# Kernel tuning notes

Measured on AMD Instinct MI355X. Metric: run time of the kernel, lower is better.

Reference implementation:

```python
import jax, jax.numpy as jnp
import numpy as np

B, S, C = 4, 1024, 1024
HD = 64          # hard-coded head dim in the module
H = C // HD      # 16 heads
ROT = 32         # RotaryEmbedding hard-codes Dim=32 (partial rotary)
EPS = 1e-4       # pnormalize eps


def pnormalize(w, parts):
    # torch: reshape(parts, -1, *w.shape[1:]); vector_norm over trailing dims;
    # alpha = sqrt(n.numel()/partitioned.numel()) = 1/sqrt(fan_in); w / (eps + alpha*n)
    p = w.reshape(parts, -1, w.shape[-1])
    n = jnp.linalg.norm(p, axis=-1, keepdims=True)
    alpha = np.sqrt(n.size / p.size)
    return (p / (EPS + alpha * n)).reshape(w.shape)


def mp_linear(x, w, parts):
    fan_in = w.shape[-1]
    return x @ (pnormalize(w, parts) / np.sqrt(fan_in)).T


def rotate_half(t):
    t1, t2 = jnp.split(t, 2, axis=-1)
    return jnp.concatenate([-t2, t1], axis=-1)


def apply_rope(t, freqs):
    return t * jnp.cos(freqs) + rotate_half(t) * jnp.sin(freqs)


def setup_inputs() -> dict:
    key = jax.random.key(0)
    k1, k2, k3, k4 = jax.random.split(key, 4)
    x = jax.random.normal(k1, (B, S, C), jnp.float32)
    w_qkv = jax.random.normal(k2, (3 * C, C), jnp.float32)   # MPLinear init: std=1
    w_out = jax.random.normal(k3, (C, C), jnp.float32)
    sink = jax.random.normal(k4, (1, 1, C), jnp.float32)
    # rotary table: RotaryEmbedding with Dim=32
    inv_freq = 1.0 / (10000.0 ** (np.arange(0, ROT, 2, dtype=np.float32) / ROT))
    t = np.arange(S, dtype=np.float32)
    freqs = np.einsum('i,j->ij', t, inv_freq)          # (S, 16)
    re = jnp.asarray(np.concatenate([freqs, freqs], axis=-1)[None, None], jnp.float32)  # (1,1,S,32)
    # causal mask over S+1 tokens (sink appended last); sink row/col fully visible
    Sf = S + 1
    m = np.tril(np.ones((Sf, Sf), dtype=bool))
    m[:, -1] = True
    m[-1, :] = True
    attn_mask = jnp.asarray(m)
    return {"x": x, "re": re, "attn_mask": attn_mask, "w_qkv": w_qkv, "w_out": w_out, "sink": sink}


def reference(x, re, attn_mask, w_qkv, w_out, sink):
    Bn, Sn, Cn = x.shape
    Hn = Cn // HD
    # append sink token
    x = jnp.concatenate([x, jnp.broadcast_to(sink, (Bn, 1, Cn))], axis=1)  # (B, S+1, C)
    qkv = mp_linear(x, w_qkv, 3)
    q, k, v = jnp.split(qkv, 3, axis=-1)
    scale = HD ** (-0.25)
    heads = lambda t: t.reshape(Bn, -1, Hn, HD).transpose(0, 2, 1, 3)  # (B,H,S+1,64)
    q, k, v = heads(q * scale), heads(k * scale), heads(v)
    # partial rotary: only non-sink tokens, only first ROT dims of head
    q_s, k_s = q[:, :, -1:], k[:, :, -1:]
    qb, kb = q[:, :, :-1], k[:, :, :-1]
    l = re.shape[-1]
    qb = jnp.concatenate([apply_rope(qb[..., :l], re), qb[..., l:]], axis=-1)
    kb = jnp.concatenate([apply_rope(kb[..., :l], re), kb[..., l:]], axis=-1)
    q = jnp.concatenate([qb, q_s], axis=2)
    k = jnp.concatenate([kb, k_s], axis=2)
    # cosine attention: unit-normalize q, k over head dim
    q = q / jnp.linalg.norm(q, axis=-1, keepdims=True)
    k = k / jnp.linalg.norm(k, axis=-1, keepdims=True)
    M = jnp.einsum('bhid,bhjd->bhij', q, k)  # (B,H,S+1,S+1)
    Sf = q.shape[2]
    M = jnp.where(attn_mask[None, None, :Sf, :Sf], M, -jnp.inf)
    A = jax.nn.softmax(M, axis=-1)
    h = jnp.einsum('bhij,bhjd->bhid', A, v)
    h = h[:, :, :-1]  # drop sink output
    h = h.transpose(0, 2, 1, 3).reshape(Bn, Sn, Cn)
    # mag_norm (no-grad magnitude matching against post-sink input x)
    desired = jax.lax.stop_gradient(jnp.mean(jnp.linalg.norm(x, axis=-1)))
    current = jax.lax.stop_gradient(jnp.mean(jnp.linalg.norm(h, axis=-1)))
    h = h * (desired / current)
    return mp_linear(h, w_out, 1)
```

## Files before the change

### kernel.cpp

```cpp
#include <hip/hip_runtime.h>
#include <hip/hip_bf16.h>
#include <cstdint>

typedef __attribute__((ext_vector_type(8))) short short8;
typedef __attribute__((ext_vector_type(4))) float f32x4;

typedef const unsigned int __attribute__((address_space(1)))* gas_ptr;
typedef unsigned int __attribute__((address_space(3)))* las_ptr;

__device__ static inline void async16(const void* g, void* l) {
  __builtin_amdgcn_global_load_lds((gas_ptr)g, (las_ptr)l, 16, 0, 0);
}

__device__ static inline unsigned short f2bf(float f) {
  union { float f; uint32_t u; } v; v.f = f;
  uint32_t u = v.u;
  uint32_t r = (u + 0x7FFFu + ((u >> 16) & 1u)) >> 16;
  return (unsigned short)r;
}
__device__ static inline float bf2f(unsigned short s) {
  union { uint32_t u; float f; } v; v.u = ((uint32_t)s) << 16; return v.f;
}

__device__ static inline float wave_sum(float v) {
  v += __shfl_xor(v, 1);  v += __shfl_xor(v, 2);  v += __shfl_xor(v, 4);
  v += __shfl_xor(v, 8);  v += __shfl_xor(v, 16); v += __shfl_xor(v, 32);
  return v;
}

#define SBAR __builtin_amdgcn_sched_barrier(0)

__global__ __launch_bounds__(256) void k_prep(const float* __restrict__ x,
    const float* __restrict__ sink, const float* __restrict__ re,
    const float* __restrict__ w_qkv, const float* __restrict__ w_out,
    unsigned short* __restrict__ Xe, unsigned short* __restrict__ Wq,
    unsigned short* __restrict__ Wo,
    float* __restrict__ ctT, float* __restrict__ stT, float* __restrict__ rowsn) {
  __shared__ float red[4];
  const int bid = blockIdx.x;
  const int tid = threadIdx.x, w = tid >> 6, l = tid & 63;
  if (bid < 4224) {
    const int row = bid;
    const int c4 = tid * 4;
    float4 v = make_float4(0.f, 0.f, 0.f, 0.f);
    if (row < 4100) {
      int b = row / 1025, s = row - b * 1025;
      const float* src = (s < 1024) ? (x + ((size_t)(b * 1024 + s)) * 1024 + c4) : (sink + c4);
      v = *(const float4*)src;
    }
    *(ushort4*)(Xe + (size_t)row * 1024 + c4) =
        make_ushort4(f2bf(v.x), f2bf(v.y), f2bf(v.z), f2bf(v.w));
    float ss = v.x * v.x + v.y * v.y + v.z * v.z + v.w * v.w;
    ss = wave_sum(ss);
    if (l == 0) red[w] = ss;
    __syncthreads();
    if (tid == 0) rowsn[row] = (row < 4100) ? sqrtf(red[0] + red[1] + red[2] + red[3]) : 0.f;
  } else if (bid < 4288) {
    int i = (bid - 4224) * 256 + tid;
    int s = i >> 4, r2 = i & 15;
    float f = re[s * 32 + r2];
    ctT[r2 * 1024 + s] = cosf(f);
    stT[r2 * 1024 + s] = sinf(f);
  } else {
    const float* W; unsigned short* E; int row;
    if (bid < 5056) { W = w_qkv; E = Wq; row = (bid - 4288) * 4 + w; }
    else            { W = w_out; E = Wo; row = (bid - 5056) * 4 + w; }
    const float* wr = W + (size_t)row * 1024;
    float4 v[4];
    float s = 0.f;
    #pragma unroll
    for (int i = 0; i < 4; ++i) {
      v[i] = *(const float4*)(wr + i * 256 + l * 4);
      s += v[i].x * v[i].x + v[i].y * v[i].y + v[i].z * v[i].z + v[i].w * v[i].w;
    }
    s = wave_sum(s);
    float inv = 1.0f / (0.0032f + sqrtf(s));
    unsigned short* er = E + (size_t)row * 1024;
    #pragma unroll
    for (int i = 0; i < 4; ++i) {
      ushort4 o = make_ushort4(f2bf(v[i].x * inv), f2bf(v[i].y * inv),
                               f2bf(v[i].z * inv), f2bf(v[i].w * inv));
      *(ushort4*)(er + i * 256 + l * 4) = o;
    }
  }
}

__global__ __launch_bounds__(256) void k_rownormC(const float* __restrict__ rowsqp,
    const float* __restrict__ rowsn, float* __restrict__ scp) {
  __shared__ float red[4];
  const int bid = blockIdx.x, t = threadIdx.x, w = t >> 6, l = t & 63;
  const int row = bid * 256 + t;
  const float4* rp = (const float4*)(rowsqp + (size_t)row * 16);
  float4 a = rp[0], b = rp[1], c = rp[2], d = rp[3];
  float s = a.x + a.y + a.z + a.w + b.x + b.y + b.z + b.w +
            c.x + c.y + c.z + c.w + d.x + d.y + d.z + d.w;
  float v = sqrtf(s);
  v = wave_sum(v);
  if (l == 0) red[w] = v;
  __syncthreads();
  if (t == 0) scp[16 + bid] = red[0] + red[1] + red[2] + red[3];
  float u = 0.f;
  for (int k = t; k < 264; k += 256) u += rowsn[bid * 264 + k];
  u = wave_sum(u);
  __syncthreads();
  if (l == 0) red[w] = u;
  __syncthreads();
  if (t == 0) scp[bid] = red[0] + red[1] + red[2] + red[3];
}

template<int EPI>
__global__ __launch_bounds__(256, 4) void k_gemm128(
    const unsigned short* __restrict__ A, const unsigned short* __restrict__ B,
    float* __restrict__ C, int N, int K, int ntn,
    unsigned short* __restrict__ Qh, unsigned short* __restrict__ Kh,
    unsigned short* __restrict__ Vt,
    const float* __restrict__ ctT, const float* __restrict__ stT,
    const float* __restrict__ scp) {
  constexpr int BM = EPI ? 128 : 64;
  constexpr int MI = BM / 32;
  __shared__ __align__(16) short SMEM[(BM + 128) * 64];
  short* Al = SMEM;
  short* Bl = SMEM + BM * 64;
  const int t = threadIdx.x, l = t & 63, w = t >> 6;
  const int r = l & 15, g = l >> 4;
  const int wm = w >> 1, wn = w & 1;
  const int nwg = gridDim.x;
  const int q = nwg >> 3, rr = nwg & 7;
  const int xcd = blockIdx.x & 7, loc = blockIdx.x >> 3;
  const int wgid = (xcd < rr ? xcd * (q + 1) : rr * (q + 1) + (xcd - rr) * q) + loc;
  const int tm = wgid / ntn, tn = wgid % ntn;
  const size_t am0 = (size_t)tm * BM, bn0 = (size_t)tn * 128;

  f32x4 acc[MI][4] = {};
  for (int kt = 0; kt < K; kt += 64) {
    __syncthreads();
    #pragma unroll
    for (int i = 0; i < BM / 32; ++i) {
      int c = i * 256 + t;
      int row = c >> 3, sch = (c & 7) ^ (row & 7);
      async16(A + (am0 + row) * (size_t)K + kt + sch * 8, Al + (i * 256 + w * 64) * 8);
    }
    #pragma unroll
    for (int i = 0; i < 4; ++i) {
      int c = i * 256 + t;
      int row = c >> 3, sch = (c & 7) ^ (row & 7);
      async16(B + (bn0 + row) * (size_t)K + kt + sch * 8, Bl + (i * 256 + w * 64) * 8);
    }
    __syncthreads();
    #pragma unroll
    for (int ks = 0; ks < 2; ++ks) {
      short8 af[MI], bfr[4];
      #pragma unroll
      for (int mi = 0; mi < MI; ++mi) {
        const int arow = wm * (MI * 16) + mi * 16 + r;
        af[mi] = *(const short8*)(Al + arow * 64 + (((ks * 4 + g) ^ (arow & 7)) << 3));
      }
      #pragma unroll
      for (int ni = 0; ni < 4; ++ni) {
        const int brow = wn * 64 + ni * 16 + r;
        bfr[ni] = *(const short8*)(Bl + brow * 64 + (((ks * 4 + g) ^ (brow & 7)) << 3));
      }
      #pragma unroll
      for (int mi = 0; mi < MI; ++mi)
        #pragma unroll
        for (int ni = 0; ni < 4; ++ni)
          acc[mi][ni] = __builtin_amdgcn_mfma_f32_16x16x32_bf16(af[mi], bfr[ni], acc[mi][ni], 0, 0, 0);
    }
  }

  if constexpr (EPI == 0) {
    float num = 0.f, den = 0.f;
    #pragma unroll
    for (int i = 0; i < 16; ++i) { num += scp[i]; den += scp[16 + i]; }
    const float ratio = (num * (1.0f / 4100.0f)) * (4096.0f / den);
    #pragma unroll
    for (int mi = 0; mi < MI; ++mi)
      #pragma unroll
      for (int ni = 0; ni < 4; ++ni)
        #pragma unroll
        for (int j = 0; j < 4; ++j) {
          size_t row = am0 + wm * (MI * 16) + mi * 16 + g * 4 + j;
          size_t col = bn0 + wn * 64 + ni * 16 + r;
          C[row * (size_t)N + col] = acc[mi][ni][j] * ratio;
        }
  } else {
    __syncthreads();
    const int head_global = tn * 2 + wn;
    const int sel = head_global >> 4;
    const int h = head_global & 15;
    const int row0 = (int)am0 + wm * 64;

    if (sel < 2) {
      unsigned short* dst = (sel == 0) ? Qh : Kh;
      #pragma unroll
      for (int mi = 0; mi < 4; ++mi) {
        const int rowb = row0 + mi * 16 + g * 4;
        const int b = rowb / 1025;
        const int s0 = rowb - b * 1025;
        float cs[4], sn[4];
        if (s0 + 3 < 1024) {
          float4 c4 = *(const float4*)(ctT + r * 1024 + s0);
          float4 s4 = *(const float4*)(stT + r * 1024 + s0);
          cs[0] = c4.x; cs[1] = c4.y; cs[2] = c4.z; cs[3] = c4.w;
          sn[0] = s4.x; sn[1] = s4.y; sn[2] = s4.z; sn[3] = s4.w;
        } else {
          #pragma unroll
          for (int j = 0; j < 4; ++j) {
            const int rj = rowb + j;
            const int bj = rj / 1025, sj = rj - bj * 1025;
            cs[j] = (sj < 1024) ? ctT[r * 1024 + sj] : 1.f;
            sn[j] = (sj < 1024) ? stT[r * 1024 + sj] : 0.f;
          }
        }
        #pragma unroll
        for (int j = 0; j < 4; ++j) {
          const int row = rowb + j;
          const int b2 = row / 1025, s = row - b2 * 1025;
          const float a0 = acc[mi][0][j], a1 = acc[mi][1][j];
          const float a2 = acc[mi][2][j], a3 = acc[mi][3][j];
          const float r0 = a0 * cs[j] - a1 * sn[j];
          const float r1 = a1 * cs[j] + a0 * sn[j];
          float nrm = r0 * r0 + r1 * r1 + a2 * a2 + a3 * a3;
          nrm += __shfl_xor(nrm, 1); nrm += __shfl_xor(nrm, 2);
          nrm += __shfl_xor(nrm, 4); nrm += __shfl_xor(nrm, 8);
          const float inv = rsqrtf(nrm);
          if (row < 4100) {
            const size_t base = ((size_t)(b2 * 16 + h) * 1088 + s) * 64 + r;
            dst[base]      = f2bf(r0 * inv);
            dst[base + 16] = f2bf(r1 * inv);
            dst[base + 32] = f2bf(a2 * inv);
            dst[base + 48] = f2bf(a3 * inv);
          }
        }
      }
    } else {
      short* vs = SMEM + w * 4096;
      #pragma unroll
      for (int mi = 0; mi < 4; ++mi) {
        const int slot = mi * 4 + g;
        #pragma unroll
        for (int ni = 0; ni < 4; ++ni) {
          const int d = ni * 16 + r;
          ushort4 pk = make_ushort4(f2bf(acc[mi][ni][0]), f2bf(acc[mi][ni][1]),
                                    f2bf(acc[mi][ni][2]), f2bf(acc[mi][ni][3]));
          *(ushort4*)(vs + d * 64 + ((slot ^ (d & 15)) << 2)) = pk;
        }
      }
      asm volatile("s_waitcnt lgkmcnt(0)" ::: "memory"); SBAR;
      #pragma unroll
      for (int ii = 0; ii < 16; ++ii) {
        const int d = ii * 4 + g;
        ushort4 vv = *(const ushort4*)(vs + d * 64 + (((r ^ (d & 15)) & 15) << 2));
        const int grow = row0 + r * 4;
        const int b0 = grow / 1025, b3 = (grow + 3) / 1025;
        if (b0 == b3 && grow + 3 < 4100) {
          const int s = grow - b0 * 1025;
          *(ushort4*)(Vt + ((size_t)(b0 * 16 + h) * 64 + d) * 1088 + s) = vv;
        } else {
          unsigned short tmp[4] = {vv.x, vv.y, vv.z, vv.w};
          for (int k2 = 0; k2 < 4; ++k2) {
            const int gr = grow + k2;
            if (gr >= 4100) break;
            const int bb = gr / 1025, ss = gr - bb * 1025;
            Vt[((size_t)(bb * 16 + h) * 64 + d) * 1088 + ss] = tmp[k2];
          }
        }
      }
    }
  }
}

__global__ __launch_bounds__(256) void k_attn(const unsigned short* __restrict__ Qh,
    const unsigned short* __restrict__ Kh, const unsigned short* __restrict__ Vt,
    unsigned short* __restrict__ Hb, float* __restrict__ rowsqp) {
  __shared__ __align__(16) short Kl[2][64 * 64];
  __shared__ __align__(16) short Vl[2][64 * 64];
  __shared__ __align__(16) short Pl[64 * 64];
  const int wid = blockIdx.x;
  const int xcd = wid & 7, jj = wid >> 3;
  const int bh = xcd + 8 * (jj & 7);
  const int p = 15 - (jj >> 3);
  const int b = bh >> 4, hh = bh & 15;
  const int t = threadIdx.x, l = t & 63, w = t >> 6;
  const int r = l & 15, g = l >> 4;
  const int qrow0 = p * 64 + w * 16;

  auto stage = [&](int buf, int kt) {
    #pragma unroll
    for (int i = 0; i < 2; ++i) {
      int c = i * 256 + t;
      int row = c >> 3, sch = (c & 7) ^ (row & 7);
      async16(Kh + ((size_t)bh * 1088 + kt * 64 + row) * 64 + sch * 8,
              Kl[buf] + (i * 256 + w * 64) * 8);
      async16(Vt + ((size_t)bh * 64 + row) * 1088 + kt * 64 + sch * 8,
              Vl[buf] + (i * 256 + w * 64) * 8);
    }
  };

  short8 qf[2];
  #pragma unroll
  for (int ks = 0; ks < 2; ++ks)
    qf[ks] = *(const short8*)(Qh + ((size_t)bh * 1088 + qrow0 + r) * 64 + ks * 32 + g * 8);
  f32x4 oacc[4] = {};
  float lsum[4] = {0.f, 0.f, 0.f, 0.f};
  stage(0, 0);
  __syncthreads();
  int cur = 0;
  for (int i = 0; i <= p; ++i) {
    if (i < p) stage(cur ^ 1, i + 1);
    const bool needmask = (i == p);
    for (int nc = 0; nc < 4; ++nc) {
      f32x4 sc = {};
      #pragma unroll
      for (int ks = 0; ks < 2; ++ks) {
        const int row = nc * 16 + r;
        const short8 kf = *(const short8*)(Kl[cur] + row * 64 + (((ks * 4 + g) ^ (row & 7)) << 3));
        sc = __builtin_amdgcn_mfma_f32_16x16x32_bf16(qf[ks], kf, sc, 0, 0, 0);
      }
      const int col = i * 64 + nc * 16 + r;
      #pragma unroll
      for (int j = 0; j < 4; ++j) {
        const int qrow = qrow0 + g * 4 + j;
        const bool valid = !needmask || (col <= qrow);
        float pv = valid ? __expf(sc[j]) : 0.0f;
        unsigned short pb = f2bf(pv);
        lsum[j] += bf2f(pb);
        const int prow = w * 16 + g * 4 + j;
        const int bir = (nc * 16 + r) * 2;
        char* pd = (char*)Pl + prow * 128 + ((((unsigned)bir >> 4) ^ (prow & 7)) << 4) + (bir & 15);
        *(short*)pd = (short)pb;
      }
    }
    #pragma unroll
    for (int ks = 0; ks < 2; ++ks) {
      const int prow = w * 16 + r;
      const short8 pf = *(const short8*)((char*)Pl + prow * 128 + (((ks * 4 + g) ^ (r & 7)) << 4));
      #pragma unroll
      for (int nd = 0; nd < 4; ++nd) {
        const int vrow = nd * 16 + r;
        const short8 vf = *(const short8*)(Vl[cur] + vrow * 64 + (((ks * 4 + g) ^ (vrow & 7)) << 3));
        oacc[nd] = __builtin_amdgcn_mfma_f32_16x16x32_bf16(pf, vf, oacc[nd], 0, 0, 0);
      }
    }
    __syncthreads();
    cur ^= 1;
  }

  float psink[4];
  {
    const unsigned short* krow = Kh + ((size_t)bh * 1088 + 1024) * 64;
    const short8 ksv0 = *(const short8*)(krow + g * 8);
    const short8 ksv1 = *(const short8*)(krow + 32 + g * 8);
    float d = 0.f;
    #pragma unroll
    for (int e = 0; e < 8; ++e)
      d += bf2f((unsigned short)qf[0][e]) * bf2f((unsigned short)ksv0[e])
         + bf2f((unsigned short)qf[1][e]) * bf2f((unsigned short)ksv1[e]);
    d += __shfl_xor(d, 16); d += __shfl_xor(d, 32);
    #pragma unroll
    for (int j = 0; j < 4; ++j)
      psink[j] = __expf(__shfl(d, (int)(g * 4 + j)));
    #pragma unroll
    for (int nd = 0; nd < 4; ++nd) {
      const float vsv = bf2f(Vt[((size_t)bh * 64 + nd * 16 + r) * 1088 + 1024]);
      #pragma unroll
      for (int j = 0; j < 4; ++j) oacc[nd][j] += psink[j] * vsv;
    }
  }

  float inv[4];
  #pragma unroll
  for (int j = 0; j < 4; ++j) {
    float v = lsum[j];
    v += __shfl_xor(v, 1); v += __shfl_xor(v, 2);
    v += __shfl_xor(v, 4); v += __shfl_xor(v, 8);
    inv[j] = 1.0f / (v + psink[j]);
  }
  #pragma unroll
  for (int j = 0; j < 4; ++j) {
    const int srow = qrow0 + g * 4 + j;
    float sq = 0.f;
    #pragma unroll
    for (int nd = 0; nd < 4; ++nd) {
      const float hv = oacc[nd][j] * inv[j];
      Hb[((size_t)(b * 1024 + srow)) * 1024 + hh * 64 + nd * 16 + r] = f2bf(hv);
      sq += hv * hv;
    }
    sq += __shfl_xor(sq, 1); sq += __shfl_xor(sq, 2);
    sq += __shfl_xor(sq, 4); sq += __shfl_xor(sq, 8);
    if (r == 0) rowsqp[(size_t)(b * 1024 + srow) * 16 + hh] = sq;
  }
}

extern "C" void kernel_launch(void* const* d_in, const int* in_sizes, int n_in,
                              void* d_out, int out_size, void* d_ws, size_t ws_size,
                              hipStream_t stream) {
  const float* x     = (const float*)d_in[0];
  const float* re    = (const float*)d_in[1];
  const float* w_qkv = (const float*)d_in[3];
  const float* w_out = (const float*)d_in[4];
  const float* sink  = (const float*)d_in[5];
  char* ws = (char*)d_ws;

  unsigned short* Wq   = (unsigned short*)(ws + 0);
  unsigned short* Wo   = (unsigned short*)(ws + 6291456);
  unsigned short* Xe   = (unsigned short*)(ws + 8388608);
  unsigned short* Hb   = (unsigned short*)(ws + 17301504);
  unsigned short* Qh   = (unsigned short*)(ws + 25690112);
  unsigned short* Kh   = (unsigned short*)(ws + 34603008);
  unsigned short* Vt   = (unsigned short*)(ws + 43515904);
  float*          ctT  = (float*)(ws + 52428800);
  float*          stT  = (float*)(ws + 52494336);
  float*          scp  = (float*)(ws + 52559872);
  float*          rowsn  = (float*)(ws + 52560384);
  float*          rowsqp = (float*)(ws + 52577792);
  float*          out  = (float*)d_out;

  k_prep<<<5312, 256, 0, stream>>>(x, sink, re, w_qkv, w_out, Xe, Wq, Wo, ctT, stT, rowsn);
  k_gemm128<1><<<33 * 24, 256, 0, stream>>>(Xe, Wq, nullptr, 3072, 1024, 24,
                                            Qh, Kh, Vt, ctT, stT, scp);
  k_attn<<<1024, 256, 0, stream>>>(Qh, Kh, Vt, Hb, rowsqp);
  k_rownormC<<<16, 256, 0, stream>>>(rowsqp, rowsn, scp);
  k_gemm128<0><<<64 * 8, 256, 0, stream>>>(Hb, Wo, out, 1024, 1024, 8,
                                           nullptr, nullptr, nullptr, ctT, stT, scp);
}
```

Before: 99.52 us.

## Process two adjacent 64-row query tiles per attention block to reuse K/V loads

Each attention workgroup now handles 128 query rows (two 64-row tiles) instead of 64, so every K/V tile staged into LDS feeds both sets of MFMAs. The grid is halved to 512 blocks, and the P scratch buffer is doubled in LDS. This is meant to halve the global-to-LDS K/V traffic and the number of barriers per query row. In exchange it uses more registers and LDS, fewer blocks run (lower occupancy and parallelism), and work is less balanced across blocks.

```diff
diff --git a/kernel.cpp b/kernel.cpp
--- a/kernel.cpp
+++ b/kernel.cpp
@@ -275,15 +275,17 @@
     unsigned short* __restrict__ Hb, float* __restrict__ rowsqp) {
   __shared__ __align__(16) short Kl[2][64 * 64];
   __shared__ __align__(16) short Vl[2][64 * 64];
-  __shared__ __align__(16) short Pl[64 * 64];
+  __shared__ __align__(16) short Pl[2][64 * 64];
   const int wid = blockIdx.x;
   const int xcd = wid & 7, jj = wid >> 3;
   const int bh = xcd + 8 * (jj & 7);
-  const int p = 15 - (jj >> 3);
+  const int qq = 7 - (jj >> 3);
   const int b = bh >> 4, hh = bh & 15;
   const int t = threadIdx.x, l = t & 63, w = t >> 6;
   const int r = l & 15, g = l >> 4;
-  const int qrow0 = p * 64 + w * 16;
+  const int rowA = qq * 128 + w * 16;
+  const int rowB = rowA + 64;
+  const int NTOT = 2 * qq + 2;
 
   auto stage = [&](int buf, int kt) {
     #pragma unroll
@@ -297,98 +299,123 @@
     }
   };
 
-  short8 qf[2];
+  short8 qfA[2], qfB[2];
   #pragma unroll
-  for (int ks = 0; ks < 2; ++ks)
-    qf[ks] = *(const short8*)(Qh + ((size_t)bh * 1088 + qrow0 + r) * 64 + ks * 32 + g * 8);
-  f32x4 oacc[4] = {};
-  float lsum[4] = {0.f, 0.f, 0.f, 0.f};
+  for (int ks = 0; ks < 2; ++ks) {
+    qfA[ks] = *(const short8*)(Qh + ((size_t)bh * 1088 + rowA + r) * 64 + ks * 32 + g * 8);
+    qfB[ks] = *(const short8*)(Qh + ((size_t)bh * 1088 + rowB + r) * 64 + ks * 32 + g * 8);
+  }
+  f32x4 oaccA[4] = {}, oaccB[4] = {};
+  float lsumA[4] = {0.f, 0.f, 0.f, 0.f}, lsumB[4] = {0.f, 0.f, 0.f, 0.f};
   stage(0, 0);
   __syncthreads();
   int cur = 0;
-  for (int i = 0; i <= p; ++i) {
-    if (i < p) stage(cur ^ 1, i + 1);
-    const bool needmask = (i == p);
+  for (int i = 0; i < NTOT; ++i) {
+    if (i + 1 < NTOT) stage(cur ^ 1, i + 1);
+    const bool actA = (i <= 2 * qq);
+    const bool mA = (i == 2 * qq), mB = (i == NTOT - 1);
     for (int nc = 0; nc < 4; ++nc) {
-      f32x4 sc = {};
+      f32x4 scA = {}, scB = {};
       #pragma unroll
       for (int ks = 0; ks < 2; ++ks) {
         const int row = nc * 16 + r;
         const short8 kf = *(const short8*)(Kl[cur] + row * 64 + (((ks * 4 + g) ^ (row & 7)) << 3));
-        sc = __builtin_amdgcn_mfma_f32_16x16x32_bf16(qf[ks], kf, sc, 0, 0, 0);
+        if (actA) scA = __builtin_amdgcn_mfma_f32_16x16x32_bf16(qfA[ks], kf, scA, 0, 0, 0);
+        scB = __builtin_amdgcn_mfma_f32_16x16x32_bf16(qfB[ks], kf, scB, 0, 0, 0);
       }
       const int col = i * 64 + nc * 16 + r;
+      const int prow = w * 16 + g * 4;
+      const int bir = (nc * 16 + r) * 2;
+      if (actA) {
+        #pragma unroll
+        for (int j = 0; j < 4; ++j) {
+          const bool valid = !mA || (col <= rowA + g * 4 + j);
+          float pv = valid ? __expf(scA[j]) : 0.0f;
+          unsigned short pb = f2bf(pv);
+          lsumA[j] += bf2f(pb);
+          char* pd = (char*)Pl[0] + (prow + j) * 128 + ((((unsigned)bir >> 4) ^ ((prow + j) & 7)) << 4) + (bir & 15);
+          *(short*)pd = (short)pb;
+        }
+      }
       #pragma unroll
       for (int j = 0; j < 4; ++j) {
-        const int qrow = qrow0 + g * 4 + j;
-        const bool valid = !needmask || (col <= qrow);
-        float pv = valid ? __expf(sc[j]) : 0.0f;
+        const bool valid = !mB || (col <= rowB + g * 4 + j);
+        float pv = valid ? __expf(scB[j]) : 0.0f;
         unsigned short pb = f2bf(pv);
-        lsum[j] += bf2f(pb);
-        const int prow = w * 16 + g * 4 + j;
-        const int bir = (nc * 16 + r) * 2;
-        char* pd = (char*)Pl + prow * 128 + ((((unsigned)bir >> 4) ^ (prow & 7)) << 4) + (bir & 15);
+        lsumB[j] += bf2f(pb);
+        char* pd = (char*)Pl[1] + (prow + j) * 128 + ((((unsigned)bir >> 4) ^ ((prow + j) & 7)) << 4) + (bir & 15);
         *(short*)pd = (short)pb;
       }
     }
     #pragma unroll
     for (int ks = 0; ks < 2; ++ks) {
       const int prow = w * 16 + r;
-      const short8 pf = *(const short8*)((char*)Pl + prow * 128 + (((ks * 4 + g) ^ (r & 7)) << 4));
+      short8 pfA{}, pfB;
+      if (actA) pfA = *(const short8*)((char*)Pl[0] + prow * 128 + (((ks * 4 + g) ^ (r & 7)) << 4));
+      pfB = *(const short8*)((char*)Pl[1] + prow * 128 + (((ks * 4 + g) ^ (r & 7)) << 4));
       #pragma unroll
       for (int nd = 0; nd < 4; ++nd) {
         const int vrow = nd * 16 + r;
         const short8 vf = *(const short8*)(Vl[cur] + vrow * 64 + (((ks * 4 + g) ^ (vrow & 7)) << 3));
-        oacc[nd] = __builtin_amdgcn_mfma_f32_16x16x32_bf16(pf, vf, oacc[nd], 0, 0, 0);
+        if (actA) oaccA[nd] = __builtin_amdgcn_mfma_f32_16x16x32_bf16(pfA, vf, oaccA[nd], 0, 0, 0);
+        oaccB[nd] = __builtin_amdgcn_mfma_f32_16x16x32_bf16(pfB, vf, oaccB[nd], 0, 0, 0);
       }
     }
     __syncthreads();
     cur ^= 1;
   }
 
-  float psink[4];
+  float psA[4], psB[4];
   {
     const unsigned short* krow = Kh + ((size_t)bh * 1088 + 1024) * 64;
     const short8 ksv0 = *(const short8*)(krow + g * 8);
     const short8 ksv1 = *(const short8*)(krow + 32 + g * 8);
-    float d = 0.f;
-    #pragma unroll
-    for (int e = 0; e < 8; ++e)
-      d += bf2f((unsigned short)qf[0][e]) * bf2f((unsigned short)ksv0[e])
-         + bf2f((unsigned short)qf[1][e]) * bf2f((unsigned short)ksv1[e]);
-    d += __shfl_xor(d, 16); d += __shfl_xor(d, 32);
-    #pragma unroll
-    for (int j = 0; j < 4; ++j)
-      psink[j] = __expf(__shfl(d, (int)(g * 4 + j)));
+    float dA = 0.f, dB = 0.f;
+    #pragma unroll
+    for (int e = 0; e < 8; ++e) {
+      const float k0 = bf2f((unsigned short)ksv0[e]), k1 = bf2f((unsigned short)ksv1[e]);
+      dA += bf2f((unsigned short)qfA[0][e]) * k0 + bf2f((unsigned short)qfA[1][e]) * k1;
+      dB += bf2f((unsigned short)qfB[0][e]) * k0 + bf2f((unsigned short)qfB[1][e]) * k1;
+    }
+    dA += __shfl_xor(dA, 16); dA += __shfl_xor(dA, 32);
+    dB += __shfl_xor(dB, 16); dB += __shfl_xor(dB, 32);
+    #pragma unroll
+    for (int j = 0; j < 4; ++j) {
+      psA[j] = __expf(__shfl(dA, (int)(g * 4 + j)));
+      psB[j] = __expf(__shfl(dB, (int)(g * 4 + j)));
+    }
     #pragma unroll
     for (int nd = 0; nd < 4; ++nd) {
       const float vsv = bf2f(Vt[((size_t)bh * 64 + nd * 16 + r) * 1088 + 1024]);
       #pragma unroll
-      for (int j = 0; j < 4; ++j) oacc[nd][j] += psink[j] * vsv;
-    }
-  }
-
-  float inv[4];
+      for (int j = 0; j < 4; ++j) { oaccA[nd][j] += psA[j] * vsv; oaccB[nd][j] += psB[j] * vsv; }
+    }
+  }
+
   #pragma unroll
-  for (int j = 0; j < 4; ++j) {
-    float v = lsum[j];
-    v += __shfl_xor(v, 1); v += __shfl_xor(v, 2);
-    v += __shfl_xor(v, 4); v += __shfl_xor(v, 8);
-    inv[j] = 1.0f / (v + psink[j]);
-  }
-  #pragma unroll
-  for (int j = 0; j < 4; ++j) {
-    const int srow = qrow0 + g * 4 + j;
-    float sq = 0.f;
-    #pragma unroll
-    for (int nd = 0; nd < 4; ++nd) {
-      const float hv = oacc[nd][j] * inv[j];
-      Hb[((size_t)(b * 1024 + srow)) * 1024 + hh * 64 + nd * 16 + r] = f2bf(hv);
-      sq += hv * hv;
-    }
-    sq += __shfl_xor(sq, 1); sq += __shfl_xor(sq, 2);
-    sq += __shfl_xor(sq, 4); sq += __shfl_xor(sq, 8);
-    if (r == 0) rowsqp[(size_t)(b * 1024 + srow) * 16 + hh] = sq;
+  for (int st2 = 0; st2 < 2; ++st2) {
+    const int qrow0 = st2 ? rowB : rowA;
+    f32x4* oacc = st2 ? oaccB : oaccA;
+    float* lsum = st2 ? lsumB : lsumA;
+    float* ps = st2 ? psB : psA;
+    #pragma unroll
+    for (int j = 0; j < 4; ++j) {
+      float v = lsum[j];
+      v += __shfl_xor(v, 1); v += __shfl_xor(v, 2);
+      v += __shfl_xor(v, 4); v += __shfl_xor(v, 8);
+      const float inv = 1.0f / (v + ps[j]);
+      const int srow = qrow0 + g * 4 + j;
+      float sq = 0.f;
+      #pragma unroll
+      for (int nd = 0; nd < 4; ++nd) {
+        const float hv = oacc[nd][j] * inv;
+        Hb[((size_t)(b * 1024 + srow)) * 1024 + hh * 64 + nd * 16 + r] = f2bf(hv);
+        sq += hv * hv;
+      }
+      sq += __shfl_xor(sq, 1); sq += __shfl_xor(sq, 2);
+      sq += __shfl_xor(sq, 4); sq += __shfl_xor(sq, 8);
+      if (r == 0) rowsqp[(size_t)(b * 1024 + srow) * 16 + hh] = sq;
+    }
   }
 }
 
@@ -419,7 +446,7 @@
   k_prep<<<5312, 256, 0, stream>>>(x, sink, re, w_qkv, w_out, Xe, Wq, Wo, ctT, stT, rowsn);
   k_gemm128<1><<<33 * 24, 256, 0, stream>>>(Xe, Wq, nullptr, 3072, 1024, 24,
                                             Qh, Kh, Vt, ctT, stT, scp);
-  k_attn<<<1024, 256, 0, stream>>>(Qh, Kh, Vt, Hb, rowsqp);
+  k_attn<<<512, 256, 0, stream>>>(Qh, Kh, Vt, Hb, rowsqp);
   k_rownormC<<<16, 256, 0, stream>>>(rowsqp, rowsn, scp);
   k_gemm128<0><<<64 * 8, 256, 0, stream>>>(Hb, Wo, out, 1024, 1024, 8,
                                            nullptr, nullptr, nullptr, ctT, stT, scp);
```

Result: slower. 107.6 us (+8.1%).
